# Kernel optimization log

Measured on AMD Instinct MI355X. Metric: run time of the kernel, lower is better.

## Reference

```python
import jax, jax.numpy as jnp
import numpy as np

K = 3
PAD = 1


def conv3x3(x, w, b):
    # x: [B,Ci,H,W], w: [Co,Ci,3,3] -> [B,Co,H,W]
    y = jax.lax.conv_general_dilated(
        x, w, window_strides=(1, 1), padding=((PAD, PAD), (PAD, PAD)),
        dimension_numbers=('NCHW', 'OIHW', 'NCHW'))
    return y + b[None, :, None, None]


def _gather(x_flat, idx):
    # x_flat: [C, H*W], idx: [K2*H*W] -> [C, K2*H*W]
    return x_flat[:, idx]


def deform_sample(x, off_x, off_y, mask):
    """Modulated deformable im2col (DCNv2, dg=1, stride=1, pad=1, dil=1).
    x: [B,C,H,W]; off_x, off_y, mask: [B,K2,H,W] -> cols [B,C,K2,H,W]."""
    B, C, H, W = x.shape
    K2 = K * K
    # static kernel-tap displacements relative to output pixel
    dy = jnp.repeat(jnp.arange(K), K) - PAD          # [K2]
    dx = jnp.tile(jnp.arange(K), K) - PAD            # [K2]
    gy = jnp.arange(H)[:, None].astype(x.dtype)      # [H,1]
    gx = jnp.arange(W)[None, :].astype(x.dtype)      # [1,W]
    ys = gy[None, None] + dy[None, :, None, None].astype(x.dtype) + off_y  # [B,K2,H,W]
    xs = gx[None, None] + dx[None, :, None, None].astype(x.dtype) + off_x
    y0 = jnp.floor(ys)
    x0 = jnp.floor(xs)
    wy1 = ys - y0
    wx1 = xs - x0
    xf = x.reshape(B, C, H * W)
    val = jnp.zeros((B, C, K2, H, W), x.dtype)
    for oy, ox in ((0, 0), (0, 1), (1, 0), (1, 1)):
        yy = y0 + oy
        xx = x0 + ox
        wgt = (wy1 if oy else 1.0 - wy1) * (wx1 if ox else 1.0 - wx1)
        valid = ((yy >= 0) & (yy < H) & (xx >= 0) & (xx < W)).astype(x.dtype)
        idx = (jnp.clip(yy, 0, H - 1) * W + jnp.clip(xx, 0, W - 1)).astype(jnp.int32)
        g = jax.vmap(_gather)(xf, idx.reshape(B, -1)).reshape(B, C, K2, H, W)
        val = val + (wgt * valid)[:, None] * g
    return val * mask[:, None]  # modulation, broadcast over C


def reference(x, feat, w_off, b_off, w_def, b_def):
    # offset/mask prediction conv (3*K2 channels), chunked as in the torch module
    om = conv3x3(feat, w_off, b_off)
    off_x, off_y, m = jnp.split(om, 3, axis=1)   # each [B,K2,H,W]
    mask = jax.nn.sigmoid(m)
    cols = deform_sample(x, off_x, off_y, mask)  # [B,C,K2,H,W]
    O = w_def.shape[0]
    out = jnp.einsum('bckhw,ock->bohw', cols, w_def.reshape(O, -1, K * K))
    out = out + b_def[None, :, None, None]
    return jax.nn.relu(out)


def setup_inputs() -> dict:
    key = jax.random.key(0)
    k1, k2, k3, k4 = jax.random.split(key, 4)
    B, C, O, H, W = 4, 64, 64, 128, 128
    K2 = K * K
    x = jax.random.normal(k1, (B, C, H, W), jnp.float32)
    feat = jax.random.normal(k2, (B, C, H, W), jnp.float32)
    # offset conv params: small init so offsets stay near zero (as in practice)
    w_off = jax.random.normal(k3, (3 * K2, C, 3, 3), jnp.float32) * 0.01
    b_off = jnp.zeros((3 * K2,), jnp.float32)
    w_def = jax.random.normal(k4, (O, C, 3, 3), jnp.float32) * (1.0 / np.sqrt(C * K2))
    b_def = jnp.zeros((O,), jnp.float32)
    return {"x": x, "feat": feat, "w_off": w_off, "b_off": b_off,
            "w_def": w_def, "b_def": b_def}
```

## Files before the change

kernel.cpp:

```cpp
#include <hip/hip_runtime.h>
#include <math.h>

#define Bn 4
#define Cn 64
#define On 64
#define Hn 128
#define Wn 128
#define HWn (Hn * Wn)

typedef __attribute__((ext_vector_type(8))) short s16x8;
typedef __attribute__((ext_vector_type(4))) float f32x4;

__device__ __forceinline__ unsigned short f2bf(float f) {
    unsigned u = __float_as_uint(f);
    u += 0x7fffu + ((u >> 16) & 1u);
    return (unsigned short)(u >> 16);
}
__device__ __forceinline__ float bf2f(unsigned short u) {
    return __uint_as_float(((unsigned)u) << 16);
}
__device__ __forceinline__ int swz(int row, int ch) {
    return row * 32 + (((ch ^ (row >> 1)) & 3) << 3);
}

__global__ __launch_bounds__(256) void transpose_all(const float* __restrict__ x,
                                                     const float* __restrict__ feat,
                                                     const float* __restrict__ wdef,
                                                     const float* __restrict__ woff,
                                                     ushort* __restrict__ xt,
                                                     ushort* __restrict__ ft,
                                                     ushort* __restrict__ wdT2,
                                                     ushort* __restrict__ woT2) {
    int t = threadIdx.x;
    if (blockIdx.z == 2) {
        int id = (blockIdx.y * gridDim.x + blockIdx.x) * 256 + t;
        if (id < 36864) {
            int c2 = id & 31, oc = (id >> 5) & 63, ks = id >> 11;
            int k = ks % 9, s = ks / 9;
            wdT2[id] = f2bf(wdef[(oc * 64 + s * 32 + c2) * 9 + k]);
        } else if (id < 55296) {
            int i2 = id - 36864;
            int c2 = i2 & 31, oc = (i2 >> 5) & 31, ks = i2 >> 10;
            int k = ks % 9, s = ks / 9;
            woT2[i2] = (oc < 27) ? f2bf(woff[(oc * 64 + s * 32 + c2) * 9 + k]) : (ushort)0;
        }
        return;
    }
    __shared__ float tile[64][65];
    const float* src = blockIdx.z ? feat : x;
    ushort* dst0 = blockIdx.z ? ft : xt;
    int b = blockIdx.y, hw0 = blockIdx.x * 64;
    int lane = t & 63, grp = t >> 6;
    const float* xb = src + (size_t)b * Cn * HWn;
#pragma unroll
    for (int i = 0; i < 16; ++i) {
        int c = grp * 16 + i;
        tile[lane][c] = xb[(size_t)c * HWn + hw0 + lane];
    }
    __syncthreads();
#pragma unroll
    for (int jj = 0; jj < 2; ++jj) {
        int px = jj * 32 + (t >> 3), ch = t & 7;
        s16x8 p;
#pragma unroll
        for (int j = 0; j < 8; ++j) p[j] = (short)f2bf(tile[px][ch * 8 + j]);
        *(s16x8*)(dst0 + ((size_t)(b * HWn + hw0 + px)) * Cn + ch * 8) = p;
    }
}

__global__ __launch_bounds__(256, 3) void off_conv_kernel(const ushort* __restrict__ ft,
                                                          const ushort* __restrict__ woT2,
                                                          const float* __restrict__ b_off,
                                                          float* __restrict__ om) {
    __shared__ __align__(16) char smem[31488];
    ushort* s_win = (ushort*)smem;
    ushort* s_wgt = (ushort*)(smem + 13056);
    float* s_out = (float*)smem;

    int t = threadIdx.x;
    int wv = t >> 6, l = t & 63;
    int q = l >> 4, r = l & 15;
    int h = blockIdx.x >> 1, wb = (blockIdx.x & 1) * 64;
    int b = blockIdx.y;
    const ushort* ft_b = ft + (size_t)b * HWn * Cn;

    f32x4 zero = {0.f, 0.f, 0.f, 0.f};
    s16x8 zz = {0, 0, 0, 0, 0, 0, 0, 0};
    f32x4 acc[2];
    acc[0] = zero; acc[1] = zero;

    for (int s = 0; s < 2; ++s) {
        for (int j = t; j < 816; j += 256) {
            int row = j / 272, rm = j - row * 272;
            int col = rm >> 2, ch = rm & 3;
            int rs = min(max(h - 1 + row, 0), Hn - 1);
            int cs = min(max(wb - 1 + col, 0), Wn - 1);
            s16x8 v = *(const s16x8*)(ft_b + (size_t)(rs * Wn + cs) * Cn + s * 32 + ch * 8);
            *(s16x8*)&s_win[swz(row * 68 + col, ch)] = v;
        }
        for (int j = t; j < 1152; j += 256) {
            int ro = j >> 2, ch = j & 3;
            s16x8 v = *(const s16x8*)(woT2 + (size_t)s * 9216 + ro * 32 + ch * 8);
            *(s16x8*)&s_wgt[swz(ro, ch)] = v;
        }
        __syncthreads();
#pragma unroll 3
        for (int k = 0; k < 9; ++k) {
            int dy = k / 3 - 1, dx = k % 3 - 1;
            int y = h + dy;
            bool yv = (y >= 0) && (y < Hn);
            int px = wv * 16 + r;
            int xx = wb + px + dx;
            bool valid = yv && (xx >= 0) && (xx < Wn);
            int lin = (dy + 1) * 68 + px + dx + 1;
            s16x8 av = *(const s16x8*)&s_win[swz(lin, q)];
            av = valid ? av : zz;
#pragma unroll
            for (int ot = 0; ot < 2; ++ot) {
                s16x8 bv = *(const s16x8*)&s_wgt[swz(k * 32 + ot * 16 + r, q)];
                acc[ot] = __builtin_amdgcn_mfma_f32_16x16x32_bf16(av, bv, acc[ot], 0, 0, 0);
            }
        }
        __syncthreads();
    }
#pragma unroll
    for (int ot = 0; ot < 2; ++ot) {
        int oc = ot * 16 + r;
        float bo = (oc < 27) ? b_off[oc] : 0.f;
#pragma unroll
        for (int reg = 0; reg < 4; ++reg) {
            int px = wv * 16 + q * 4 + reg;
            float v = acc[ot][reg] + bo;
            if (oc >= 18 && oc < 27) v = 1.f / (1.f + __expf(-v));
            s_out[oc * 68 + px] = v;
        }
    }
    __syncthreads();
    for (int idx = t; idx < 27 * 64; idx += 256) {
        int o = idx >> 6, px = idx & 63;
        om[((size_t)b * 27 + o) * HWn + h * Wn + wb + px] = s_out[o * 68 + px];
    }
}

__global__ __launch_bounds__(256, 3) void mega_kernel(const ushort* __restrict__ xt,
                                                      const ushort* __restrict__ wdT2,
                                                      const float* __restrict__ om,
                                                      const float* __restrict__ b_def,
                                                      float* __restrict__ out) {
    __shared__ __align__(16) char smem[28672];
    ushort* s_win = (ushort*)smem;
    float* s_out = (float*)smem;

    int t = threadIdx.x;
    int wv = t >> 6, l = t & 63;
    int q = l >> 4, r = l & 15;
    int blk = (blockIdx.x & 7) * 128 + (blockIdx.x >> 3);
    int b = blk >> 8;
    int gi = blk & 255;
    int h = (gi >> 2) << 1;
    int wbase = (gi & 3) << 5;
    int rowoff = wv >> 1, pxh = wv & 1;
    int hrow = h + rowoff;
    int pxi = pxh * 16 + r;
    float pxif = (float)pxi;
    float rowofff = (float)rowoff;
    const ushort* xt_b = xt + (size_t)b * HWn * Cn;

#pragma unroll
    for (int i = 0; i < 7; ++i) {
        int jb = i * 256 + wv * 64;
        int j = jb + l;
        int lin = j >> 3, slot = j & 7;
        int linc = min(lin, 215);
        int cidx = (slot - lin) & 7;
        int row = linc / 36, col = linc - row * 36;
        int rs = min(max(h - 2 + row, 0), Hn - 1);
        int cs = min(max(wbase - 2 + col, 0), Wn - 1);
        const ushort* gp = xt_b + (size_t)(rs * Wn + cs) * Cn + cidx * 8;
        __builtin_amdgcn_global_load_lds(
            (const __attribute__((address_space(1))) unsigned int*)gp,
            (__attribute__((address_space(3))) unsigned int*)(s_win + (size_t)jb * 8),
            16, 0, 0);
    }

    const float* om_b = om + ((size_t)b * 27) * HWn + hrow * Wn + wbase + pxi;
    float omv[27];
#pragma unroll
    for (int o = 0; o < 27; ++o) omv[o] = om_b[(size_t)o * HWn];

    bool okp = true;
#pragma unroll
    for (int k = 0; k < 9; ++k) {
        float uy = (float)(k / 3 - 1) + omv[9 + k];
        float ux = pxif + (float)(k % 3 - 1) + omv[k];
        okp = okp && (uy >= -2.f - rowofff) && (uy < 3.f - rowofff)
                  && (ux >= -2.f) && (ux < 33.f);
    }
    int fast = __all(okp) ? 1 : 0;

    __syncthreads();

    f32x4 zero = {0.f, 0.f, 0.f, 0.f};
    f32x4 acc[4];
    acc[0] = zero; acc[1] = zero; acc[2] = zero; acc[3] = zero;

    if (fast) {
#pragma unroll 3
        for (int k = 0; k < 9; ++k) {
            float uy = (float)(k / 3 - 1) + omv[9 + k];
            float ux = pxif + (float)(k % 3 - 1) + omv[k];
            float mv = omv[18 + k];
            float y0f = floorf(uy), x0f = floorf(ux);
            float fy = uy - y0f, fx = ux - x0f;
            int iy = (int)y0f + 2 + rowoff;
            int ix = (int)x0f + 2;
            int yab = hrow + (int)y0f, xab = wbase + (int)x0f;
            bool vy0 = (yab >= 0) && (yab < Hn);
            bool vy1 = (yab + 1 >= 0) && (yab + 1 < Hn);
            bool vx0 = (xab >= 0) && (xab < Wn);
            bool vx1 = (xab + 1 >= 0) && (xab + 1 < Wn);
            float g0 = (vy0 && vx0) ? (1.f - fy) * (1.f - fx) * mv : 0.f;
            float g1 = (vy0 && vx1) ? (1.f - fy) * fx * mv : 0.f;
            float g2 = (vy1 && vx0) ? fy * (1.f - fx) * mv : 0.f;
            float g3 = (vy1 && vx1) ? fy * fx * mv : 0.f;
            int l0 = iy * 36 + ix, l1 = l0 + 1, l2 = l0 + 36, l3 = l0 + 37;
            s16x8 bw[2][4];
#pragma unroll
            for (int s = 0; s < 2; ++s)
#pragma unroll
                for (int ot = 0; ot < 4; ++ot)
                    bw[s][ot] = *(const s16x8*)(wdT2 + (size_t)s * 18432
                                                + (size_t)(k * 64 + ot * 16 + r) * 32 + q * 8);
            s16x8 af[2];
#pragma unroll
            for (int s = 0; s < 2; ++s) {
                int c = s * 4 + q;
                s16x8 q0 = *(const s16x8*)&s_win[l0 * 64 + (((c + l0) & 7) << 3)];
                s16x8 q1 = *(const s16x8*)&s_win[l1 * 64 + (((c + l1) & 7) << 3)];
                s16x8 q2 = *(const s16x8*)&s_win[l2 * 64 + (((c + l2) & 7) << 3)];
                s16x8 q3 = *(const s16x8*)&s_win[l3 * 64 + (((c + l3) & 7) << 3)];
                s16x8 p;
#pragma unroll
                for (int j = 0; j < 8; ++j) {
                    float rr = g0 * bf2f((unsigned short)q0[j]) + g1 * bf2f((unsigned short)q1[j])
                             + g2 * bf2f((unsigned short)q2[j]) + g3 * bf2f((unsigned short)q3[j]);
                    p[j] = (short)f2bf(rr);
                }
                af[s] = p;
            }
#pragma unroll
            for (int s = 0; s < 2; ++s)
#pragma unroll
                for (int ot = 0; ot < 4; ++ot)
                    acc[ot] = __builtin_amdgcn_mfma_f32_16x16x32_bf16(af[s], bw[s][ot], acc[ot], 0, 0, 0);
        }
    } else {
#pragma unroll 1
        for (int k = 0; k < 9; ++k) {
            float ys = (float)(hrow + k / 3 - 1) + omv[9 + k];
            float xs = (float)(wbase + pxi + k % 3 - 1) + omv[k];
            float mv = omv[18 + k];
            float y0f = floorf(ys), x0f = floorf(xs);
            float fy = ys - y0f, fx = xs - x0f;
            int y0 = (int)y0f, x0 = (int)x0f;
            float g[4];
            int a[4];
#pragma unroll
            for (int n = 0; n < 4; ++n) {
                int yy = y0 + (n >> 1), xx = x0 + (n & 1);
                bool valid = (yy >= 0) && (yy < Hn) && (xx >= 0) && (xx < Wn);
                float wgt = ((n >> 1) ? fy : 1.f - fy) * ((n & 1) ? fx : 1.f - fx) * mv;
                g[n] = valid ? wgt : 0.f;
                int yc = min(max(yy, 0), Hn - 1), xc = min(max(xx, 0), Wn - 1);
                a[n] = (yc * Wn + xc) * Cn;
            }
#pragma unroll
            for (int s = 0; s < 2; ++s) {
                int c = s * 32 + q * 8;
                s16x8 q0 = *(const s16x8*)(xt_b + a[0] + c);
                s16x8 q1 = *(const s16x8*)(xt_b + a[1] + c);
                s16x8 q2 = *(const s16x8*)(xt_b + a[2] + c);
                s16x8 q3 = *(const s16x8*)(xt_b + a[3] + c);
                s16x8 af;
#pragma unroll
                for (int j = 0; j < 8; ++j) {
                    float rr = g[0] * bf2f((unsigned short)q0[j]) + g[1] * bf2f((unsigned short)q1[j])
                             + g[2] * bf2f((unsigned short)q2[j]) + g[3] * bf2f((unsigned short)q3[j]);
                    af[j] = (short)f2bf(rr);
                }
#pragma unroll
                for (int ot = 0; ot < 4; ++ot) {
                    s16x8 bv = *(const s16x8*)(wdT2 + (size_t)s * 18432
                                               + (size_t)(k * 64 + ot * 16 + r) * 32 + q * 8);
                    acc[ot] = __builtin_amdgcn_mfma_f32_16x16x32_bf16(af, bv, acc[ot], 0, 0, 0);
                }
            }
        }
    }
    __syncthreads();

#pragma unroll
    for (int ot = 0; ot < 4; ++ot) {
        int oc = ot * 16 + r;
        float bv = b_def[oc];
        f32x4 vv;
#pragma unroll
        for (int reg = 0; reg < 4; ++reg) vv[reg] = fmaxf(acc[ot][reg] + bv, 0.f);
        *(f32x4*)&s_out[oc * 68 + rowoff * 32 + pxh * 16 + q * 4] = vv;
    }
    __syncthreads();
    {
        int px = t & 63, og = t >> 6;
        int rg = h + (px >> 5);
        float* ob = out + ((size_t)b * On) * HWn + rg * Wn + wbase + (px & 31);
#pragma unroll
        for (int j = 0; j < 16; ++j) {
            int oc = og * 16 + j;
            ob[(size_t)oc * HWn] = s_out[oc * 68 + px];
        }
    }
}

extern "C" void kernel_launch(void* const* d_in, const int* in_sizes, int n_in,
                              void* d_out, int out_size, void* d_ws, size_t ws_size,
                              hipStream_t stream) {
    const float* x = (const float*)d_in[0];
    const float* feat = (const float*)d_in[1];
    const float* w_off = (const float*)d_in[2];
    const float* b_off = (const float*)d_in[3];
    const float* w_def = (const float*)d_in[4];
    const float* b_def = (const float*)d_in[5];
    float* out = (float*)d_out;

    char* ws = (char*)d_ws;
    ushort* xt = (ushort*)ws;
    ushort* ft = (ushort*)(ws + 8388608);
    ushort* wdT2 = (ushort*)(ws + 16777216);
    ushort* woT2 = (ushort*)(ws + 16850944);
    float* om = (float*)(ws + 16887808);

    hipLaunchKernelGGL(transpose_all, dim3(HWn / 64, Bn, 3), dim3(256), 0, stream,
                       x, feat, w_def, w_off, xt, ft, wdT2, woT2);
    hipLaunchKernelGGL(off_conv_kernel, dim3(Hn * 2, Bn), dim3(256), 0, stream,
                       ft, woT2, b_off, om);
    hipLaunchKernelGGL(mega_kernel, dim3((Bn * HWn) / 64), dim3(256), 0, stream,
                       xt, wdT2, om, b_def, out);
}
```

Measured before the change: 128.3 us.

## Load offset-conv window via direct global-to-LDS and read weights from global

The offset conv kernel now fills the full 64-channel input window in one pass using global_load_lds direct-to-LDS transfers with a new XOR-rotated layout, instead of two staged register round-trips over channel halves. Weight tiles are no longer staged in shared memory and are read straight from global/L2 per MFMA. This removes one barrier pair and the register hop, and the smaller LDS footprint allows a higher occupancy hint (4 blocks). The tradeoff is repeated global weight loads in the inner loop, which may add latency if they miss cache.

```diff
diff --git a/kernel.cpp b/kernel.cpp
--- a/kernel.cpp
+++ b/kernel.cpp
@@ -18,9 +18,6 @@
 }
 __device__ __forceinline__ float bf2f(unsigned short u) {
     return __uint_as_float(((unsigned)u) << 16);
-}
-__device__ __forceinline__ int swz(int row, int ch) {
-    return row * 32 + (((ch ^ (row >> 1)) & 3) << 3);
 }
 
 __global__ __launch_bounds__(256) void transpose_all(const float* __restrict__ x,
@@ -68,13 +65,12 @@
     }
 }
 
-__global__ __launch_bounds__(256, 3) void off_conv_kernel(const ushort* __restrict__ ft,
+__global__ __launch_bounds__(256, 4) void off_conv_kernel(const ushort* __restrict__ ft,
                                                           const ushort* __restrict__ woT2,
                                                           const float* __restrict__ b_off,
                                                           float* __restrict__ om) {
-    __shared__ __align__(16) char smem[31488];
+    __shared__ __align__(16) char smem[26624];
     ushort* s_win = (ushort*)smem;
-    ushort* s_wgt = (ushort*)(smem + 13056);
     float* s_out = (float*)smem;
 
     int t = threadIdx.x;
@@ -84,61 +80,71 @@
     int b = blockIdx.y;
     const ushort* ft_b = ft + (size_t)b * HWn * Cn;
 
+#pragma unroll
+    for (int i = 0; i < 7; ++i) {
+        int jb = i * 256 + wv * 64;
+        if (jb < 1664) {
+            int j = jb + l;
+            int lin = j >> 3, slot = j & 7;
+            int linc = min(lin, 203);
+            int cidx = (slot - lin) & 7;
+            int row = linc / 68, col = linc - row * 68;
+            int rs = min(max(h - 1 + row, 0), Hn - 1);
+            int cs = min(max(wb - 1 + col, 0), Wn - 1);
+            const ushort* gp = ft_b + (size_t)(rs * Wn + cs) * Cn + cidx * 8;
+            __builtin_amdgcn_global_load_lds(
+                (const __attribute__((address_space(1))) unsigned int*)gp,
+                (__attribute__((address_space(3))) unsigned int*)(s_win + (size_t)jb * 8),
+                16, 0, 0);
+        }
+    }
+    __syncthreads();
+
     f32x4 zero = {0.f, 0.f, 0.f, 0.f};
     s16x8 zz = {0, 0, 0, 0, 0, 0, 0, 0};
     f32x4 acc[2];
     acc[0] = zero; acc[1] = zero;
 
-    for (int s = 0; s < 2; ++s) {
-        for (int j = t; j < 816; j += 256) {
-            int row = j / 272, rm = j - row * 272;
-            int col = rm >> 2, ch = rm & 3;
-            int rs = min(max(h - 1 + row, 0), Hn - 1);
-            int cs = min(max(wb - 1 + col, 0), Wn - 1);
-            s16x8 v = *(const s16x8*)(ft_b + (size_t)(rs * Wn + cs) * Cn + s * 32 + ch * 8);
-            *(s16x8*)&s_win[swz(row * 68 + col, ch)] = v;
-        }
-        for (int j = t; j < 1152; j += 256) {
-            int ro = j >> 2, ch = j & 3;
-            s16x8 v = *(const s16x8*)(woT2 + (size_t)s * 9216 + ro * 32 + ch * 8);
-            *(s16x8*)&s_wgt[swz(ro, ch)] = v;
-        }
-        __syncthreads();
+    int px = wv * 16 + r;
 #pragma unroll 3
-        for (int k = 0; k < 9; ++k) {
-            int dy = k / 3 - 1, dx = k % 3 - 1;
-            int y = h + dy;
-            bool yv = (y >= 0) && (y < Hn);
-            int px = wv * 16 + r;
-            int xx = wb + px + dx;
-            bool valid = yv && (xx >= 0) && (xx < Wn);
-            int lin = (dy + 1) * 68 + px + dx + 1;
-            s16x8 av = *(const s16x8*)&s_win[swz(lin, q)];
+    for (int k = 0; k < 9; ++k) {
+        int dy = k / 3 - 1, dx = k % 3 - 1;
+        int y = h + dy;
+        bool yv = (y >= 0) && (y < Hn);
+        int xx = wb + px + dx;
+        bool valid = yv && (xx >= 0) && (xx < Wn);
+        int lin = (dy + 1) * 68 + px + dx + 1;
+#pragma unroll
+        for (int s = 0; s < 2; ++s) {
+            int c = s * 4 + q;
+            s16x8 av = *(const s16x8*)&s_win[lin * 64 + (((c + lin) & 7) << 3)];
             av = valid ? av : zz;
 #pragma unroll
             for (int ot = 0; ot < 2; ++ot) {
-                s16x8 bv = *(const s16x8*)&s_wgt[swz(k * 32 + ot * 16 + r, q)];
+                s16x8 bv = *(const s16x8*)(woT2 + (size_t)s * 9216
+                                           + (size_t)(k * 32 + ot * 16 + r) * 32 + q * 8);
                 acc[ot] = __builtin_amdgcn_mfma_f32_16x16x32_bf16(av, bv, acc[ot], 0, 0, 0);
             }
         }
-        __syncthreads();
-    }
+    }
+    __syncthreads();
+
 #pragma unroll
     for (int ot = 0; ot < 2; ++ot) {
         int oc = ot * 16 + r;
         float bo = (oc < 27) ? b_off[oc] : 0.f;
 #pragma unroll
         for (int reg = 0; reg < 4; ++reg) {
-            int px = wv * 16 + q * 4 + reg;
+            int p = wv * 16 + q * 4 + reg;
             float v = acc[ot][reg] + bo;
             if (oc >= 18 && oc < 27) v = 1.f / (1.f + __expf(-v));
-            s_out[oc * 68 + px] = v;
+            s_out[oc * 68 + p] = v;
         }
     }
     __syncthreads();
     for (int idx = t; idx < 27 * 64; idx += 256) {
-        int o = idx >> 6, px = idx & 63;
-        om[((size_t)b * 27 + o) * HWn + h * Wn + wb + px] = s_out[o * 68 + px];
+        int o = idx >> 6, p = idx & 63;
+        om[((size_t)b * 27 + o) * HWn + h * Wn + wb + p] = s_out[o * 68 + p];
     }
 }
 
```

New measurement: 131.5 us. 2.5% more time.
